# Optimization experiments

Hardware: AMD Instinct MI355X
Metric: run time of the kernel (lower is better)

## Reference

```python
import jax, jax.numpy as jnp
import numpy as np

P = 32    # cardinality (number of parallel paths)
C = 256   # block input/output channels
D = 4     # bottleneck width per path
EPS = 1e-3  # Keras BatchNormalization default epsilon


def setup_inputs() -> dict:
    key = jax.random.key(0)
    ks = jax.random.split(key, 24)
    def nrm(k, shape, s=0.05):
        return jax.random.normal(k, shape, dtype=jnp.float32) * s
    inp = {}
    inp["x"] = jax.random.normal(ks[0], (8, 56, 56, C), dtype=jnp.float32)
    # conv weights/biases, stacked over the path axis P
    inp["W1"] = nrm(ks[1], (P, C, D))          # 1x1 conv C->4
    inp["B1"] = nrm(ks[2], (P, D))
    inp["W2"] = nrm(ks[3], (P, 3, 3, D, D))    # 3x3 conv 4->4 (HWIO)
    inp["B2"] = nrm(ks[4], (P, D))
    inp["W3"] = nrm(ks[5], (P, D, C))          # 1x1 conv 4->256
    inp["B3"] = nrm(ks[6], (P, C))
    # BatchNorm (inference): gamma, beta, moving mean, moving var per stage
    inp["G1"]  = 1.0 + nrm(ks[7], (P, D));  inp["Be1"] = nrm(ks[8], (P, D))
    inp["M1"]  = nrm(ks[9], (P, D));        inp["V1"]  = 1.0 + 0.1 * jax.random.uniform(ks[10], (P, D), dtype=jnp.float32)
    inp["G2"]  = 1.0 + nrm(ks[11], (P, D)); inp["Be2"] = nrm(ks[12], (P, D))
    inp["M2"]  = nrm(ks[13], (P, D));       inp["V2"]  = 1.0 + 0.1 * jax.random.uniform(ks[14], (P, D), dtype=jnp.float32)
    inp["G3"]  = 1.0 + nrm(ks[15], (P, C)); inp["Be3"] = nrm(ks[16], (P, C))
    inp["M3"]  = nrm(ks[17], (P, C));       inp["V3"]  = 1.0 + 0.1 * jax.random.uniform(ks[18], (P, C), dtype=jnp.float32)
    return inp


def _bn(x, g, b, m, v):
    # inference batch-norm: affine over channel axis
    return g * (x - m) * jax.lax.rsqrt(v + EPS) + b


def _path(x, w1, b1, g1, be1, m1, v1, w2, b2, g2, be2, m2, v2, w3, b3, g3, be3, m3, v3):
    h = jnp.einsum('nhwc,cd->nhwd', x, w1) + b1            # 1x1 conv C->D
    h = jax.nn.relu(_bn(h, g1, be1, m1, v1))
    h = jax.lax.conv_general_dilated(
        h, w2, window_strides=(1, 1), padding='SAME',
        dimension_numbers=('NHWC', 'HWIO', 'NHWC')) + b2   # 3x3 conv D->D
    h = jax.nn.relu(_bn(h, g2, be2, m2, v2))
    h = jnp.einsum('nhwd,dc->nhwc', h, w3) + b3            # 1x1 conv D->C
    h = jax.nn.relu(_bn(h, g3, be3, m3, v3))
    return h  # Dropout(0.2) is identity at inference


def reference(x, W1, B1, G1, Be1, M1, V1, W2, B2, G2, Be2, M2, V2, W3, B3, G3, Be3, M3, V3):
    # vmap over the 32 cardinality paths; x is shared (in_axes=None)
    paths = jax.vmap(_path, in_axes=(None,) + (0,) * 18)(
        x, W1, B1, G1, Be1, M1, V1, W2, B2, G2, Be2, M2, V2, W3, B3, G3, Be3, M3, V3)
    return jax.nn.relu(paths.sum(axis=0) + x)
```

## Files before the change

kernel.cpp:

```cpp
#include <hip/hip_runtime.h>

#define BATCH 8
#define HH 56
#define WW 56
#define NPOS (BATCH*HH*WW)
#define C 256
#define P 32
#define D 4
#define J 128
#define EPS 1e-3f
#define H1S 136
#define H2S 136

typedef __attribute__((ext_vector_type(8))) short bf16x8_t;
typedef __attribute__((ext_vector_type(4))) float f32x4_t;

__device__ __forceinline__ unsigned short f2bf(float f) {
    union { float f; unsigned int i; } v; v.f = f;
    unsigned int r = v.i + 0x7fffu + ((v.i >> 16) & 1u);
    return (unsigned short)(r >> 16);
}
__device__ __forceinline__ uint2 pack4_trunc(float4 v) {
    uint2 r;
    r.x = __builtin_amdgcn_perm(__float_as_uint(v.y), __float_as_uint(v.x), 0x07060302u);
    r.y = __builtin_amdgcn_perm(__float_as_uint(v.w), __float_as_uint(v.z), 0x07060302u);
    return r;
}

__global__ __launch_bounds__(256) void fold_params(
    const float* __restrict__ W1, const float* __restrict__ B1,
    const float* __restrict__ W2, const float* __restrict__ B2,
    const float* __restrict__ W3, const float* __restrict__ B3,
    const float* __restrict__ G1, const float* __restrict__ Be1,
    const float* __restrict__ M1, const float* __restrict__ V1,
    const float* __restrict__ G2, const float* __restrict__ Be2,
    const float* __restrict__ M2, const float* __restrict__ V2,
    const float* __restrict__ G3, const float* __restrict__ Be3,
    const float* __restrict__ M3, const float* __restrict__ V3,
    unsigned short* __restrict__ W1bf, float* __restrict__ b1f,
    float* __restrict__ b2t,
    unsigned short* __restrict__ WB, unsigned short* __restrict__ zb,
    unsigned short* __restrict__ wbd)
{
    int idx = blockIdx.x * 256 + threadIdx.x;

    if (idx < C*J) {
        int j = idx >> 8, c = idx & 255;
        int p = j >> 2, d = j & 3;
        float s = G1[j] * rsqrtf(V1[j] + EPS);
        W1bf[idx] = f2bf(W1[(p*C + c)*D + d] * s);
        return;
    }
    idx -= C*J;
    if (idx < J) {
        float s = G1[idx] * rsqrtf(V1[idx] + EPS);
        b1f[idx] = B1[idx] * s + Be1[idx] - M1[idx] * s;
        return;
    }
    idx -= J;
    if (idx < J) {
        int do_ = idx >> 5, p = idx & 31;
        int j = p*4 + do_;
        float s = G2[j] * rsqrtf(V2[j] + EPS);
        b2t[idx] = B2[j] * s + Be2[j] - M2[j] * s;
        return;
    }
    idx -= J;
    if (idx < P*C*8) {
        int s8 = idx & 7;
        int c = (idx >> 3) & 255;
        int p = idx >> 11;
        float sc = G3[p*C + c] * rsqrtf(V3[p*C + c] + EPS);
        float v = 0.f;
        if (s8 < 4)       v = W3[(p*D + s8)*C + c] * sc;
        else if (s8 == 4) v = B3[p*C + c] * sc + Be3[p*C + c] - M3[p*C + c] * sc;
        WB[idx] = f2bf(v);
        return;
    }
    idx -= P*C*8;
    if (idx < 8) { zb[idx] = 0; return; }
    idx -= 8;
    if (idx < 8*5*16*32) {
        int k = idx & 31;
        int rest = idx >> 5;
        int n = rest & 15;
        int rest2 = rest >> 4;
        int tp = rest2 % 5;
        int pg = rest2 / 5;
        int tap = tp*2 + (k >> 4);
        int pk = (k >> 2) & 3, di = k & 3;
        int pn = n >> 2, do_ = n & 3;
        float v = 0.f;
        if (pk == pn && tap <= 8) {
            int p = pg*4 + pn;
            int j = p*4 + do_;
            float s = G2[j] * rsqrtf(V2[j] + EPS);
            v = W2[((p*9 + tap)*4 + di)*4 + do_] * s;
        }
        wbd[idx] = f2bf(v);
        return;
    }
}

__global__ __launch_bounds__(256, 4) void fused_all(
    const float* __restrict__ x, const unsigned short* __restrict__ W1bf,
    const float* __restrict__ wsf,
    const unsigned short* __restrict__ WB,
    const unsigned short* __restrict__ zb,
    const unsigned short* __restrict__ wbd,
    float* __restrict__ out)
{
    __shared__ unsigned short xs[36*256];
    __shared__ unsigned short h1L[36*H1S];
    __shared__ unsigned short h2s[16*H2S];
    __shared__ float sw[256];

    const int tid = threadIdx.x;
    int bid = blockIdx.x;
    int wg = (bid & 7) * 196 + (bid >> 3);
    const int xb = wg % 14;  wg /= 14;
    const int yb = wg % 14;  const int b = wg / 14;
    const int wid = tid >> 6, l = tid & 63, l15 = l & 15, quad = l >> 4;
    const int j0w = wid * 32;

    if (tid < 256) {  }
    if (tid < 256) sw[tid] = wsf[tid];
    const float* b1s = sw;
    const float* bs  = sw + 128;

#pragma unroll
    for (int it = 0; it < 5; ++it) {
        int idx = it*256 + tid;
        int pos = idx >> 5, g = idx & 31;
        if (pos < 36) {
            int hy = (pos*43) >> 8, hx = pos - hy*6;
            int gy = yb*4 + hy - 1, gx = xb*4 + hx - 1;
            uint4 st; st.x = 0u; st.y = 0u; st.z = 0u; st.w = 0u;
            if (gy >= 0 && gy < HH && gx >= 0 && gx < WW) {
                const float* xp = &x[(size_t)((b*HH + gy)*WW + gx) * C + g*8];
                float4 v0 = *(const float4*)xp;
                float4 v1 = *(const float4*)(xp + 4);
                uint2 p0 = pack4_trunc(v0), p1 = pack4_trunc(v1);
                st.x = p0.x; st.y = p0.y; st.z = p1.x; st.w = p1.y;
            }
            *(uint4*)&xs[pos*256 + ((g ^ (pos & 7)) * 8)] = st;
        }
    }
    __syncthreads();

    union bu { uint4 u; bf16x8_t v; };
#pragma unroll
    for (int jf = 0; jf < 2; ++jf) {
        bu aw[8];
        const int wrow = j0w + jf*16 + l15;
#pragma unroll
        for (int kc = 0; kc < 8; ++kc)
            aw[kc].u = *(const uint4*)&W1bf[wrow*C + kc*32 + quad*8];
#pragma unroll
        for (int mt = 0; mt < 3; ++mt) {
            const int row = mt*16 + l15;
            const int rrow = (row < 36) ? row : 0;
            int hy = (row*43) >> 8;
            int hx = row - hy*6;
            int gy = yb*4 + hy - 1, gx = xb*4 + hx - 1;
            const bool valid = (row < 36) & (gy >= 0) & (gy < HH) & (gx >= 0) & (gx < WW);
            const unsigned mask = valid ? 0xFFFFFFFFu : 0u;
            f32x4_t acc = (f32x4_t){0.f,0.f,0.f,0.f};
#pragma unroll
            for (int kc = 0; kc < 8; ++kc) {
                int g = (kc*4 + quad) ^ (rrow & 7);
                bf16x8_t bb = *(const bf16x8_t*)&xs[rrow*256 + g*8];
                acc = __builtin_amdgcn_mfma_f32_16x16x32_bf16(aw[kc].v, bb, acc, 0, 0, 0);
            }
            if (row < 36) {
                int jb = j0w + jf*16 + quad*4;
                float4 bias = *(const float4*)&b1s[jb];
                float v0 = fmaxf(acc[0] + bias.x, 0.f);
                float v1 = fmaxf(acc[1] + bias.y, 0.f);
                float v2 = fmaxf(acc[2] + bias.z, 0.f);
                float v3 = fmaxf(acc[3] + bias.w, 0.f);
                uint2 o;
                o.x = ((unsigned int)f2bf(v0) | ((unsigned int)f2bf(v1) << 16)) & mask;
                o.y = ((unsigned int)f2bf(v2) | ((unsigned int)f2bf(v3) << 16)) & mask;
                *(uint2*)&h1L[row*H1S + jb] = o;
            }
        }
    }

    {
        const int pos = l15, py = pos >> 2, px = pos & 3;
#pragma unroll
        for (int ig = 0; ig < 2; ++ig) {
            const int pg = wid*2 + ig;
            const int pD = pg*4 + (l15 >> 2), doD = l15 & 3;
            const float bias = bs[doD*32 + pD];
            f32x4_t cacc = (f32x4_t){bias, bias, bias, bias};
#pragma unroll
            for (int tp = 0; tp < 5; ++tp) {
                int tap = tp*2 + (quad >> 1);
                if (tap > 8) tap = 8;
                int ky = (tap*11) >> 5;
                int kx = tap - ky*3;
                int hp = (py + ky)*6 + px + kx;
                bf16x8_t av = *(const bf16x8_t*)&h1L[hp*H1S + pg*16 + (quad & 1)*8];
                bf16x8_t bv = *(const bf16x8_t*)&wbd[(((pg*5 + tp)*16 + l15) << 5) + quad*8];
                cacc = __builtin_amdgcn_mfma_f32_16x16x32_bf16(av, bv, cacc, 0, 0, 0);
            }
#pragma unroll
            for (int r = 0; r < 4; ++r)
                h2s[(quad*4 + r)*H2S + pg*16 + l15] = f2bf(fmaxf(cacc[r], 0.f));
        }
    }
    __syncthreads();

    const int cb = wid * 64;
    const unsigned short* wbp;
    int pstr, cstr;
    if (quad == 0) {
        wbp = &WB[((size_t)(cb + l15)) * 8];
        pstr = C * 8;
        cstr = 16 * 8;
    } else {
        wbp = zb;
        pstr = 0; cstr = 0;
    }

    const f32x4_t zero = (f32x4_t){0.f, 0.f, 0.f, 0.f};
    f32x4_t dacc[4];
#pragma unroll
    for (int ct = 0; ct < 4; ++ct) dacc[ct] = zero;
    const unsigned int one = 0x3f80u;

#pragma unroll 2
    for (int pp = 0; pp < 16; ++pp) {
        uint4 h0 = *(const uint4*)&h2s[l15*H2S + pp*8];
        union au { unsigned int u[4]; bf16x8_t v; };
        au A0, A1;
        A0.u[0] = h0.x; A0.u[1] = h0.y; A0.u[2] = one; A0.u[3] = 0u;
        A1.u[0] = h0.z; A1.u[1] = h0.w; A1.u[2] = one; A1.u[3] = 0u;
        const unsigned short* pb0 = wbp + pp*2*pstr;
        const unsigned short* pb1 = pb0 + pstr;
#pragma unroll
        for (int ct = 0; ct < 4; ++ct) {
            union bu2 { uint4 u; bf16x8_t v; } B0, B1;
            B0.u = *(const uint4*)(pb0 + ct*cstr);
            B1.u = *(const uint4*)(pb1 + ct*cstr);
            f32x4_t z0 = __builtin_amdgcn_mfma_f32_16x16x32_bf16(A0.v, B0.v, zero, 0, 0, 0);
            f32x4_t z1 = __builtin_amdgcn_mfma_f32_16x16x32_bf16(A1.v, B1.v, zero, 0, 0, 0);
#pragma unroll
            for (int r = 0; r < 4; ++r)
                dacc[ct][r] += fmaxf(z0[r], 0.f) + fmaxf(z1[r], 0.f);
        }
    }

#pragma unroll
    for (int r = 0; r < 4; ++r) {
        int nl = quad*4 + r;
        int gy = yb*4 + (nl >> 2), gx = xb*4 + (nl & 3);
        size_t n = (size_t)((b*HH + gy)*WW + gx);
        const float* xr = &x[n*C + cb + l15];
        float* orow = &out[n*C + cb + l15];
#pragma unroll
        for (int ct = 0; ct < 4; ++ct) {
            float v = dacc[ct][r] + xr[ct*16];
            orow[ct*16] = fmaxf(v, 0.f);
        }
    }
}

extern "C" void kernel_launch(void* const* d_in, const int* in_sizes, int n_in,
                              void* d_out, int out_size, void* d_ws, size_t ws_size,
                              hipStream_t stream) {
    const float* x  = (const float*)d_in[0];
    const float* W1 = (const float*)d_in[1];
    const float* B1 = (const float*)d_in[2];
    const float* W2 = (const float*)d_in[3];
    const float* B2 = (const float*)d_in[4];
    const float* W3 = (const float*)d_in[5];
    const float* B3 = (const float*)d_in[6];
    const float* G1 = (const float*)d_in[7];
    const float* Be1= (const float*)d_in[8];
    const float* M1 = (const float*)d_in[9];
    const float* V1 = (const float*)d_in[10];
    const float* G2 = (const float*)d_in[11];
    const float* Be2= (const float*)d_in[12];
    const float* M2 = (const float*)d_in[13];
    const float* V2 = (const float*)d_in[14];
    const float* G3 = (const float*)d_in[15];
    const float* Be3= (const float*)d_in[16];
    const float* M3 = (const float*)d_in[17];
    const float* V3 = (const float*)d_in[18];

    char* wsb = (char*)d_ws;
    unsigned short* W1bf = (unsigned short*)(wsb + 0);
    unsigned short* WB   = (unsigned short*)(wsb + 65536);
    float*          b1f  = (float*)(wsb + 196608);
    float*          b2t  = (float*)(wsb + 197120);
    unsigned short* zb   = (unsigned short*)(wsb + 197632);
    unsigned short* wbd  = (unsigned short*)(wsb + 197648);
    const float*    wsf  = (const float*)(wsb + 196608);

    const int fold_tasks = C*J + J + J + P*C*8 + 8 + 8*5*16*32;
    fold_params<<<(fold_tasks + 255)/256, 256, 0, stream>>>(
        W1, B1, W2, B2, W3, B3, G1, Be1, M1, V1, G2, Be2, M2, V2,
        G3, Be3, M3, V3, W1bf, b1f, b2t, WB, zb, wbd);

    fused_all<<<8*14*14, 256, 0, stream>>>(x, W1bf, wsf, WB, zb, wbd,
                                           (float*)d_out);
}
```

Measured before the change: 167.5 us.

## Process two adjacent tiles per block and prefetch next tile's input

Each workgroup now handles two horizontally adjacent 4x4 output tiles, halving the grid. While the first tile's 1x1 and 3x3 stages run, the second tile's input halo is loaded from global memory into registers, then packed to bf16 into shared memory after a barrier. The aim is to hide global load latency behind MFMA work and amortise per-block setup. In exchange it raises register pressure, adds barriers, and reduces the number of concurrent blocks available to hide latency.

```diff
diff --git a/kernel.cpp b/kernel.cpp
--- a/kernel.cpp
+++ b/kernel.cpp
@@ -116,15 +116,15 @@
     __shared__ float sw[256];
 
     const int tid = threadIdx.x;
-    int bid = blockIdx.x;
-    int wg = (bid & 7) * 196 + (bid >> 3);
-    const int xb = wg % 14;  wg /= 14;
-    const int yb = wg % 14;  const int b = wg / 14;
+    const int bid = blockIdx.x;
+    const int b   = bid & 7;
+    const int k   = bid >> 3;
+    const int yb  = k / 7;
+    const int xb0 = (k % 7) * 2;
     const int wid = tid >> 6, l = tid & 63, l15 = l & 15, quad = l >> 4;
     const int j0w = wid * 32;
 
-    if (tid < 256) {  }
-    if (tid < 256) sw[tid] = wsf[tid];
+    sw[tid] = wsf[tid];
     const float* b1s = sw;
     const float* bs  = sw + 128;
 
@@ -134,7 +134,7 @@
         int pos = idx >> 5, g = idx & 31;
         if (pos < 36) {
             int hy = (pos*43) >> 8, hx = pos - hy*6;
-            int gy = yb*4 + hy - 1, gx = xb*4 + hx - 1;
+            int gy = yb*4 + hy - 1, gx = xb0*4 + hx - 1;
             uint4 st; st.x = 0u; st.y = 0u; st.z = 0u; st.w = 0u;
             if (gy >= 0 && gy < HH && gx >= 0 && gx < WW) {
                 const float* xp = &x[(size_t)((b*HH + gy)*WW + gx) * C + g*8];
@@ -144,71 +144,6 @@
                 st.x = p0.x; st.y = p0.y; st.z = p1.x; st.w = p1.y;
             }
             *(uint4*)&xs[pos*256 + ((g ^ (pos & 7)) * 8)] = st;
-        }
-    }
-    __syncthreads();
-
-    union bu { uint4 u; bf16x8_t v; };
-#pragma unroll
-    for (int jf = 0; jf < 2; ++jf) {
-        bu aw[8];
-        const int wrow = j0w + jf*16 + l15;
-#pragma unroll
-        for (int kc = 0; kc < 8; ++kc)
-            aw[kc].u = *(const uint4*)&W1bf[wrow*C + kc*32 + quad*8];
-#pragma unroll
-        for (int mt = 0; mt < 3; ++mt) {
-            const int row = mt*16 + l15;
-            const int rrow = (row < 36) ? row : 0;
-            int hy = (row*43) >> 8;
-            int hx = row - hy*6;
-            int gy = yb*4 + hy - 1, gx = xb*4 + hx - 1;
-            const bool valid = (row < 36) & (gy >= 0) & (gy < HH) & (gx >= 0) & (gx < WW);
-            const unsigned mask = valid ? 0xFFFFFFFFu : 0u;
-            f32x4_t acc = (f32x4_t){0.f,0.f,0.f,0.f};
-#pragma unroll
-            for (int kc = 0; kc < 8; ++kc) {
-                int g = (kc*4 + quad) ^ (rrow & 7);
-                bf16x8_t bb = *(const bf16x8_t*)&xs[rrow*256 + g*8];
-                acc = __builtin_amdgcn_mfma_f32_16x16x32_bf16(aw[kc].v, bb, acc, 0, 0, 0);
-            }
-            if (row < 36) {
-                int jb = j0w + jf*16 + quad*4;
-                float4 bias = *(const float4*)&b1s[jb];
-                float v0 = fmaxf(acc[0] + bias.x, 0.f);
-                float v1 = fmaxf(acc[1] + bias.y, 0.f);
-                float v2 = fmaxf(acc[2] + bias.z, 0.f);
-                float v3 = fmaxf(acc[3] + bias.w, 0.f);
-                uint2 o;
-                o.x = ((unsigned int)f2bf(v0) | ((unsigned int)f2bf(v1) << 16)) & mask;
-                o.y = ((unsigned int)f2bf(v2) | ((unsigned int)f2bf(v3) << 16)) & mask;
-                *(uint2*)&h1L[row*H1S + jb] = o;
-            }
-        }
-    }
-
-    {
-        const int pos = l15, py = pos >> 2, px = pos & 3;
-#pragma unroll
-        for (int ig = 0; ig < 2; ++ig) {
-            const int pg = wid*2 + ig;
-            const int pD = pg*4 + (l15 >> 2), doD = l15 & 3;
-            const float bias = bs[doD*32 + pD];
-            f32x4_t cacc = (f32x4_t){bias, bias, bias, bias};
-#pragma unroll
-            for (int tp = 0; tp < 5; ++tp) {
-                int tap = tp*2 + (quad >> 1);
-                if (tap > 8) tap = 8;
-                int ky = (tap*11) >> 5;
-                int kx = tap - ky*3;
-                int hp = (py + ky)*6 + px + kx;
-                bf16x8_t av = *(const bf16x8_t*)&h1L[hp*H1S + pg*16 + (quad & 1)*8];
-                bf16x8_t bv = *(const bf16x8_t*)&wbd[(((pg*5 + tp)*16 + l15) << 5) + quad*8];
-                cacc = __builtin_amdgcn_mfma_f32_16x16x32_bf16(av, bv, cacc, 0, 0, 0);
-            }
-#pragma unroll
-            for (int r = 0; r < 4; ++r)
-                h2s[(quad*4 + r)*H2S + pg*16 + l15] = f2bf(fmaxf(cacc[r], 0.f));
         }
     }
     __syncthreads();
@@ -224,47 +159,153 @@
         wbp = zb;
         pstr = 0; cstr = 0;
     }
-
+    const unsigned int one = 0x3f80u;
     const f32x4_t zero = (f32x4_t){0.f, 0.f, 0.f, 0.f};
-    f32x4_t dacc[4];
-#pragma unroll
-    for (int ct = 0; ct < 4; ++ct) dacc[ct] = zero;
-    const unsigned int one = 0x3f80u;
+
+    float4 pf0[5], pf1[5];
+
+#pragma unroll
+    for (int t = 0; t < 2; ++t) {
+        const int xbt = xb0 + t;
+
+        union bu { uint4 u; bf16x8_t v; };
+#pragma unroll
+        for (int jf = 0; jf < 2; ++jf) {
+            bu aw[8];
+            const int wrow = j0w + jf*16 + l15;
+#pragma unroll
+            for (int kc = 0; kc < 8; ++kc)
+                aw[kc].u = *(const uint4*)&W1bf[wrow*C + kc*32 + quad*8];
+#pragma unroll
+            for (int mt = 0; mt < 3; ++mt) {
+                const int row = mt*16 + l15;
+                const int rrow = (row < 36) ? row : 0;
+                int hy = (row*43) >> 8;
+                int hx = row - hy*6;
+                int gy = yb*4 + hy - 1, gx = xbt*4 + hx - 1;
+                const bool valid = (row < 36) & (gy >= 0) & (gy < HH) & (gx >= 0) & (gx < WW);
+                const unsigned mask = valid ? 0xFFFFFFFFu : 0u;
+                f32x4_t acc = (f32x4_t){0.f,0.f,0.f,0.f};
+#pragma unroll
+                for (int kc = 0; kc < 8; ++kc) {
+                    int g = (kc*4 + quad) ^ (rrow & 7);
+                    bf16x8_t bb = *(const bf16x8_t*)&xs[rrow*256 + g*8];
+                    acc = __builtin_amdgcn_mfma_f32_16x16x32_bf16(aw[kc].v, bb, acc, 0, 0, 0);
+                }
+                if (row < 36) {
+                    int jb = j0w + jf*16 + quad*4;
+                    float4 bias = *(const float4*)&b1s[jb];
+                    float v0 = fmaxf(acc[0] + bias.x, 0.f);
+                    float v1 = fmaxf(acc[1] + bias.y, 0.f);
+                    float v2 = fmaxf(acc[2] + bias.z, 0.f);
+                    float v3 = fmaxf(acc[3] + bias.w, 0.f);
+                    uint2 o;
+                    o.x = ((unsigned int)f2bf(v0) | ((unsigned int)f2bf(v1) << 16)) & mask;
+                    o.y = ((unsigned int)f2bf(v2) | ((unsigned int)f2bf(v3) << 16)) & mask;
+                    *(uint2*)&h1L[row*H1S + jb] = o;
+                }
+            }
+        }
+
+        if (t == 0) {
+#pragma unroll
+            for (int it = 0; it < 5; ++it) {
+                int idx = it*256 + tid;
+                int pos = idx >> 5, g = idx & 31;
+                pf0[it] = (float4){0.f,0.f,0.f,0.f};
+                pf1[it] = (float4){0.f,0.f,0.f,0.f};
+                if (pos < 36) {
+                    int hy = (pos*43) >> 8, hx = pos - hy*6;
+                    int gy = yb*4 + hy - 1, gx = (xb0+1)*4 + hx - 1;
+                    if (gy >= 0 && gy < HH && gx >= 0 && gx < WW) {
+                        const float* xp = &x[(size_t)((b*HH + gy)*WW + gx) * C + g*8];
+                        pf0[it] = *(const float4*)xp;
+                        pf1[it] = *(const float4*)(xp + 4);
+                    }
+                }
+            }
+        }
+
+        {
+            const int pos = l15, py = pos >> 2, px = pos & 3;
+#pragma unroll
+            for (int ig = 0; ig < 2; ++ig) {
+                const int pg = wid*2 + ig;
+                const int pD = pg*4 + (l15 >> 2), doD = l15 & 3;
+                const float bias = bs[doD*32 + pD];
+                f32x4_t cacc = (f32x4_t){bias, bias, bias, bias};
+#pragma unroll
+                for (int tp = 0; tp < 5; ++tp) {
+                    int tap = tp*2 + (quad >> 1);
+                    if (tap > 8) tap = 8;
+                    int ky = (tap*11) >> 5;
+                    int kx = tap - ky*3;
+                    int hp = (py + ky)*6 + px + kx;
+                    bf16x8_t av = *(const bf16x8_t*)&h1L[hp*H1S + pg*16 + (quad & 1)*8];
+                    bf16x8_t bv = *(const bf16x8_t*)&wbd[(((pg*5 + tp)*16 + l15) << 5) + quad*8];
+                    cacc = __builtin_amdgcn_mfma_f32_16x16x32_bf16(av, bv, cacc, 0, 0, 0);
+                }
+#pragma unroll
+                for (int r = 0; r < 4; ++r)
+                    h2s[(quad*4 + r)*H2S + pg*16 + l15] = f2bf(fmaxf(cacc[r], 0.f));
+            }
+        }
+        __syncthreads();
+
+        if (t == 0) {
+#pragma unroll
+            for (int it = 0; it < 5; ++it) {
+                int idx = it*256 + tid;
+                int pos = idx >> 5, g = idx & 31;
+                if (pos < 36) {
+                    uint2 p0 = pack4_trunc(pf0[it]), p1 = pack4_trunc(pf1[it]);
+                    uint4 st; st.x = p0.x; st.y = p0.y; st.z = p1.x; st.w = p1.y;
+                    *(uint4*)&xs[pos*256 + ((g ^ (pos & 7)) * 8)] = st;
+                }
+            }
+        }
+
+        f32x4_t dacc[4];
+#pragma unroll
+        for (int ct = 0; ct < 4; ++ct) dacc[ct] = zero;
 
 #pragma unroll 2
-    for (int pp = 0; pp < 16; ++pp) {
-        uint4 h0 = *(const uint4*)&h2s[l15*H2S + pp*8];
-        union au { unsigned int u[4]; bf16x8_t v; };
-        au A0, A1;
-        A0.u[0] = h0.x; A0.u[1] = h0.y; A0.u[2] = one; A0.u[3] = 0u;
-        A1.u[0] = h0.z; A1.u[1] = h0.w; A1.u[2] = one; A1.u[3] = 0u;
-        const unsigned short* pb0 = wbp + pp*2*pstr;
-        const unsigned short* pb1 = pb0 + pstr;
-#pragma unroll
-        for (int ct = 0; ct < 4; ++ct) {
-            union bu2 { uint4 u; bf16x8_t v; } B0, B1;
-            B0.u = *(const uint4*)(pb0 + ct*cstr);
-            B1.u = *(const uint4*)(pb1 + ct*cstr);
-            f32x4_t z0 = __builtin_amdgcn_mfma_f32_16x16x32_bf16(A0.v, B0.v, zero, 0, 0, 0);
-            f32x4_t z1 = __builtin_amdgcn_mfma_f32_16x16x32_bf16(A1.v, B1.v, zero, 0, 0, 0);
-#pragma unroll
-            for (int r = 0; r < 4; ++r)
-                dacc[ct][r] += fmaxf(z0[r], 0.f) + fmaxf(z1[r], 0.f);
-        }
-    }
-
-#pragma unroll
-    for (int r = 0; r < 4; ++r) {
-        int nl = quad*4 + r;
-        int gy = yb*4 + (nl >> 2), gx = xb*4 + (nl & 3);
-        size_t n = (size_t)((b*HH + gy)*WW + gx);
-        const float* xr = &x[n*C + cb + l15];
-        float* orow = &out[n*C + cb + l15];
-#pragma unroll
-        for (int ct = 0; ct < 4; ++ct) {
-            float v = dacc[ct][r] + xr[ct*16];
-            orow[ct*16] = fmaxf(v, 0.f);
-        }
+        for (int pp = 0; pp < 16; ++pp) {
+            uint4 h0 = *(const uint4*)&h2s[l15*H2S + pp*8];
+            union au { unsigned int u[4]; bf16x8_t v; };
+            au A0, A1;
+            A0.u[0] = h0.x; A0.u[1] = h0.y; A0.u[2] = one; A0.u[3] = 0u;
+            A1.u[0] = h0.z; A1.u[1] = h0.w; A1.u[2] = one; A1.u[3] = 0u;
+            const unsigned short* pb0 = wbp + pp*2*pstr;
+            const unsigned short* pb1 = pb0 + pstr;
+#pragma unroll
+            for (int ct = 0; ct < 4; ++ct) {
+                union bu2 { uint4 u; bf16x8_t v; } B0, B1;
+                B0.u = *(const uint4*)(pb0 + ct*cstr);
+                B1.u = *(const uint4*)(pb1 + ct*cstr);
+                f32x4_t z0 = __builtin_amdgcn_mfma_f32_16x16x32_bf16(A0.v, B0.v, zero, 0, 0, 0);
+                f32x4_t z1 = __builtin_amdgcn_mfma_f32_16x16x32_bf16(A1.v, B1.v, zero, 0, 0, 0);
+#pragma unroll
+                for (int r = 0; r < 4; ++r)
+                    dacc[ct][r] += fmaxf(z0[r], 0.f) + fmaxf(z1[r], 0.f);
+            }
+        }
+
+#pragma unroll
+        for (int r = 0; r < 4; ++r) {
+            int nl = quad*4 + r;
+            int gy = yb*4 + (nl >> 2), gx = xbt*4 + (nl & 3);
+            size_t n = (size_t)((b*HH + gy)*WW + gx);
+            const float* xr = &x[n*C + cb + l15];
+            float* orow = &out[n*C + cb + l15];
+#pragma unroll
+            for (int ct = 0; ct < 4; ++ct) {
+                float v = dacc[ct][r] + xr[ct*16];
+                orow[ct*16] = fmaxf(v, 0.f);
+            }
+        }
+
+        if (t == 0) __syncthreads();
     }
 }
 
@@ -305,6 +346,6 @@
         W1, B1, W2, B2, W3, B3, G1, Be1, M1, V1, G2, Be2, M2, V2,
         G3, Be3, M3, V3, W1bf, b1f, b2t, WB, zb, wbd);
 
-    fused_all<<<8*14*14, 256, 0, stream>>>(x, W1bf, wsf, WB, zb, wbd,
-                                           (float*)d_out);
-}
+    fused_all<<<784, 256, 0, stream>>>(x, W1bf, wsf, WB, zb, wbd,
+                                       (float*)d_out);
+}
```

Result: slower. 191.4 us (+14.2%).
